# Kernel optimization log

Measured on AMD Instinct MI355X. Metric: run time of the kernel, lower is better.

Reference implementation:

```python
import jax, jax.numpy as jnp
import numpy as np

B, LX, LM, D = 4, 512, 512, 256

def setup_inputs() -> dict:
    key = jax.random.key(0)
    ks = jax.random.split(key, 7)
    s = 1.0 / np.sqrt(D)
    return {
        "x": jax.random.normal(ks[0], (B, LX, D), jnp.float32),
        "memory": jax.random.normal(ks[1], (B, LM, D), jnp.float32),
        "memory_mask": jax.random.randint(ks[2], (B, LM), 0, 2, jnp.int32),
        "W1": jax.random.normal(ks[3], (D, D), jnp.float32) * s,
        "b1": jax.random.normal(ks[4], (D,), jnp.float32) * s,
        "W2": jax.random.normal(ks[5], (D, D), jnp.float32) * s,
        "Wt": jax.random.normal(ks[6], (D,), jnp.float32) * s,
    }

def reference(x, memory, memory_mask, W1, b1, W2, Wt):
    # item1: (B, Lx, D); item2: (B, Lm, D)
    item1 = jnp.einsum("bxd,ed->bxe", x, W1) + b1
    item2 = jnp.einsum("bmd,ed->bme", memory, W2)
    # additive attention: tanh of broadcast sum, then reduce D to scalar logit
    item = item1[:, :, None, :] + item2[:, None, :, :]  # (B, Lx, Lm, D)
    S_logit = jnp.einsum("bxmd,d->bxm", jnp.tanh(item), Wt)
    S_logit = jnp.where(memory_mask[:, None, :] == 0, jnp.float32(-10000.0), S_logit)
    return S_logit
```

## Files before the change

### kernel.cpp

```cpp
#include <hip/hip_runtime.h>

namespace {

constexpr int B = 4, LX = 512, LM = 512, D = 256;
constexpr float KSCALE = 2.8853900817779268f;
constexpr float CLAMP = 7.5f;

typedef __attribute__((ext_vector_type(8))) short short8;
typedef __attribute__((ext_vector_type(4))) float f32x4;
typedef __attribute__((ext_vector_type(2))) float f32x2;

__device__ __forceinline__ unsigned bfbits(float f) {
    unsigned u = __float_as_uint(f);
    u += 0x7FFFu + ((u >> 16) & 1u);
    return u >> 16;
}
__device__ __forceinline__ int pack2(float a, float b) {
    return (int)(bfbits(a) | (bfbits(b) << 16));
}
__device__ __forceinline__ f32x2 up2(unsigned u) {
    f32x2 r;
    r.x = __uint_as_float(u << 16);
    r.y = __uint_as_float(u & 0xFFFF0000u);
    return r;
}
__device__ __forceinline__ unsigned permb(unsigned hi, unsigned lo, unsigned sel) {
    return __builtin_amdgcn_perm(hi, lo, sel);
}

__global__ __launch_bounds__(256) void proj_mfma(
    const float* __restrict__ x, const float* __restrict__ mem,
    const float* __restrict__ W1, const float* __restrict__ b1v,
    const float* __restrict__ W2,
    unsigned short* __restrict__ E1h, unsigned short* __restrict__ E2h)
{
    const int tid = threadIdx.x;
    const int m0c = blockIdx.x * 32;
    const int e0  = blockIdx.y * 64;
    const int z   = m0c >= 2048;
    const int r0  = z ? (m0c - 2048) : m0c;
    const float* __restrict__ A = (z ? mem : x) + (size_t)r0 * D;
    const float* __restrict__ W = z ? W2 : W1;

    __shared__ short sA[32][40];
    __shared__ short sW[64][40];

    const int wid = tid >> 6, lane = tid & 63;
    const int lr = lane & 15, quad = lane >> 4;
    const int g   = wid & 1;
    const int cg0 = (wid >> 1) * 2;
    const int srA = tid >> 3;
    const int scA = (tid & 7) * 4;

    f32x4 acc0 = {0.f, 0.f, 0.f, 0.f};
    f32x4 acc1 = {0.f, 0.f, 0.f, 0.f};

    for (int kc = 0; kc < D; kc += 32) {
        float4 av = *(const float4*)&A[(size_t)srA * D + kc + scA];
        float4 w0 = *(const float4*)&W[(size_t)(e0 + srA) * D + kc + scA];
        float4 w1 = *(const float4*)&W[(size_t)(e0 + 32 + srA) * D + kc + scA];
        __syncthreads();
        *(int2*)&sA[srA][scA]      = make_int2(pack2(av.x, av.y), pack2(av.z, av.w));
        *(int2*)&sW[srA][scA]      = make_int2(pack2(w0.x, w0.y), pack2(w0.z, w0.w));
        *(int2*)&sW[srA + 32][scA] = make_int2(pack2(w1.x, w1.y), pack2(w1.z, w1.w));
        __syncthreads();
        short8 af  = *(const short8*)&sA[g * 16 + lr][quad * 8];
        short8 bf0 = *(const short8*)&sW[cg0 * 16 + lr][quad * 8];
        short8 bf1 = *(const short8*)&sW[cg0 * 16 + 16 + lr][quad * 8];
        acc0 = __builtin_amdgcn_mfma_f32_16x16x32_bf16(af, bf0, acc0, 0, 0, 0);
        acc1 = __builtin_amdgcn_mfma_f32_16x16x32_bf16(af, bf1, acc1, 0, 0, 0);
    }

    const float bias0 = z ? 0.f : b1v[e0 + cg0 * 16 + lr];
    const float bias1 = z ? 0.f : b1v[e0 + cg0 * 16 + 16 + lr];
    const int ec0 = e0 + cg0 * 16 + lr;
#pragma unroll
    for (int reg = 0; reg < 4; ++reg) {
        const int pair = quad * 4 + reg;
        float a0 = KSCALE * (acc0[reg] + bias0);
        float a1 = KSCALE * (acc1[reg] + bias1);
        a0 = fminf(fmaxf(a0, -CLAMP), CLAMP);
        a1 = fminf(fmaxf(a1, -CLAMP), CLAMP);
        const unsigned short e0b = (unsigned short)bfbits(__builtin_amdgcn_exp2f(a0));
        const unsigned short e1b = (unsigned short)bfbits(__builtin_amdgcn_exp2f(a1));
        if (!z) {
            const size_t base = (size_t)((r0 >> 5) * 16 + pair) * 256;
            E1h[(base + ec0) * 2 + g]      = e0b;
            E1h[(base + ec0 + 16) * 2 + g] = e1b;
        } else {
            const int row = r0 + g * 16 + pair;
            E2h[(size_t)row * 256 + ec0]      = e0b;
            E2h[(size_t)row * 256 + ec0 + 16] = e1b;
        }
    }
}

constexpr int RS = 268;
constexpr int C1 = 136;

__global__ __launch_bounds__(256, 4) void tanh_score_kernel(
    const unsigned* __restrict__ E1p, const unsigned* __restrict__ E2u,
    const float* __restrict__ Wt, const int* __restrict__ mask,
    float* __restrict__ out)
{
    const int tid = threadIdx.x;
    const int b   = blockIdx.z;
    const int yb  = blockIdx.y;
    const int T   = yb >> 1;
    const int p0  = (yb & 1) * 8;
    const int bx  = blockIdx.x;

    __shared__ unsigned sA[8 * RS];
    __shared__ unsigned sB[16 * RS];
    __shared__ int scid[LM];
    __shared__ int smsk[LM];
    __shared__ float4 sRed[128];

    const int lane = tid & 63;
    const int wid  = tid >> 6;

    int mvv[8];
#pragma unroll
    for (int c = 0; c < 8; ++c) mvv[c] = mask[b * LM + c * 64 + lane];
    int count = 0, mcount = 0;
#pragma unroll
    for (int c = 0; c < 8; ++c) {
        const bool bit = mvv[c] != 0;
        const unsigned long long bal = __ballot(bit);
        const unsigned long long lt  = (1ull << lane) - 1ull;
        const int pre  = __popcll(bal & lt);
        const int prem = __popcll(~bal & lt);
        if (wid == 0) {
            if (bit) scid[count + pre]   = c * 64 + lane;
            else     smsk[mcount + prem] = c * 64 + lane;
        }
        const int pc = __popcll(bal);
        count  += pc;
        mcount += 64 - pc;
    }

    {
        const int rA = tid >> 5, q2 = tid & 31;
        const unsigned* g =
            E1p + (size_t)((b * 16 + T) * 16 + p0 + rA) * 256 + q2 * 8;
        const int off = rA * RS + q2 * 8 + (q2 >= 16 ? 8 : 0);
        *(uint4*)&sA[off]     = *(const uint4*)(g);
        *(uint4*)&sA[off + 4] = *(const uint4*)(g + 4);
    }

    float sumW = 0.f;
#pragma unroll
    for (int i = 0; i < 256; i += 4) {
        const float4 w = *(const float4*)&Wt[i];
        sumW += (w.x + w.y) + (w.z + w.w);
    }

    __syncthreads();

    const int tx = tid & 15;
    const int ty = (tid >> 4) & 7;
    const int h  = tid >> 7;
    const int hb = h * 128;
    const int ho = h * C1;
    const f32x2 one2 = {1.f, 1.f};

#define SPL(s)  ((f32x2){(s), (s)})
#define FMA2(A_, B_, C_) __builtin_elementwise_fma((A_), (B_), (C_))
#define OCT(BX, accv) { \
    const f32x2 T0 = FMA2(a_[0], BX(0), one2), T1 = FMA2(a_[1], BX(1), one2); \
    const f32x2 T2 = FMA2(a_[2], BX(2), one2), T3 = FMA2(a_[3], BX(3), one2); \
    const f32x2 T4 = FMA2(a_[4], BX(4), one2), T5 = FMA2(a_[5], BX(5), one2); \
    const f32x2 T6 = FMA2(a_[6], BX(6), one2), T7 = FMA2(a_[7], BX(7), one2); \
    const f32x2 L0 = T0 * T1, L1 = T2 * T3, L2 = T4 * T5, L3 = T6 * T7;       \
    const f32x2 Q0 = L0 * L1, Q1 = L2 * L3;                                   \
    const f32x2 den = Q0 * Q1;                                                \
    const f32x2 n0 = FMA2(SPL(wv[0]), T1, SPL(wv[1]) * T0);                   \
    const f32x2 n1 = FMA2(SPL(wv[2]), T3, SPL(wv[3]) * T2);                   \
    const f32x2 n2 = FMA2(SPL(wv[4]), T5, SPL(wv[5]) * T4);                   \
    const f32x2 n3 = FMA2(SPL(wv[6]), T7, SPL(wv[7]) * T6);                   \
    const f32x2 u0 = FMA2(n0, L1, n1 * L0), u1 = FMA2(n2, L3, n3 * L2);       \
    const f32x2 N  = FMA2(u0, Q1, u1 * Q0);                                   \
    f32x2 r; r.x = __builtin_amdgcn_rcpf(den.x);                              \
             r.y = __builtin_amdgcn_rcpf(den.y);                              \
    (accv) = FMA2(N, r, (accv)); }
#define BP(i)  (p_[i])
#define BPS(i) (__builtin_shufflevector(p_[i], p_[i], 1, 0))

    for (int s = bx; s < 16; s += 8) {
        const int m0 = s * 32;
        if (m0 >= count) break;

        {
            const int rB = tid >> 4, q = tid & 15;
            const int clo = min(m0 + rB, count - 1);
            const int chi = min(m0 + rB + 16, count - 1);
            const unsigned* rlo = E2u + (size_t)(b * LM + scid[clo]) * 128 + q * 8;
            const unsigned* rhi = E2u + (size_t)(b * LM + scid[chi]) * 128 + q * 8;
            const uint4 Lo0 = *(const uint4*)(rlo);
            const uint4 Lo1 = *(const uint4*)(rlo + 4);
            const uint4 Hi0 = *(const uint4*)(rhi);
            const uint4 Hi1 = *(const uint4*)(rhi + 4);
            const int ob = rB * RS + q * 16 + (q >= 8 ? 8 : 0);
            uint4 P;
            P.x = permb(Hi0.x, Lo0.x, 0x05040100u); P.y = permb(Hi0.x, Lo0.x, 0x07060302u);
            P.z = permb(Hi0.y, Lo0.y, 0x05040100u); P.w = permb(Hi0.y, Lo0.y, 0x07060302u);
            *(uint4*)&sB[ob] = P;
            P.x = permb(Hi0.z, Lo0.z, 0x05040100u); P.y = permb(Hi0.z, Lo0.z, 0x07060302u);
            P.z = permb(Hi0.w, Lo0.w, 0x05040100u); P.w = permb(Hi0.w, Lo0.w, 0x07060302u);
            *(uint4*)&sB[ob + 4] = P;
            P.x = permb(Hi1.x, Lo1.x, 0x05040100u); P.y = permb(Hi1.x, Lo1.x, 0x07060302u);
            P.z = permb(Hi1.y, Lo1.y, 0x05040100u); P.w = permb(Hi1.y, Lo1.y, 0x07060302u);
            *(uint4*)&sB[ob + 8] = P;
            P.x = permb(Hi1.z, Lo1.z, 0x05040100u); P.y = permb(Hi1.z, Lo1.z, 0x07060302u);
            P.z = permb(Hi1.w, Lo1.w, 0x05040100u); P.w = permb(Hi1.w, Lo1.w, 0x07060302u);
            *(uint4*)&sB[ob + 12] = P;
        }
        __syncthreads();

        f32x2 accs = {0.f, 0.f}, accw = {0.f, 0.f};
#pragma unroll 1
        for (int d = 0; d < 128; d += 8) {
            const uint4 ua0 = *(const uint4*)&sA[ty * RS + ho + d];
            const uint4 ua1 = *(const uint4*)&sA[ty * RS + ho + d + 4];
            const uint4 ub0 = *(const uint4*)&sB[tx * RS + ho + d];
            const uint4 ub1 = *(const uint4*)&sB[tx * RS + ho + d + 4];
            const float4 w0 = *(const float4*)&Wt[hb + d];
            const float4 w1 = *(const float4*)&Wt[hb + d + 4];

            const f32x2 a_[8] = {up2(ua0.x), up2(ua0.y), up2(ua0.z), up2(ua0.w),
                                 up2(ua1.x), up2(ua1.y), up2(ua1.z), up2(ua1.w)};
            const f32x2 p_[8] = {up2(ub0.x), up2(ub0.y), up2(ub0.z), up2(ub0.w),
                                 up2(ub1.x), up2(ub1.y), up2(ub1.z), up2(ub1.w)};
            const float wv[8] = {w0.x, w0.y, w0.z, w0.w, w1.x, w1.y, w1.z, w1.w};

            OCT(BP,  accs)
            OCT(BPS, accw)
        }

        if (h) sRed[ty * 16 + tx] = make_float4(accs.x, accs.y, accw.x, accw.y);
        __syncthreads();
        if (!h) {
            const float4 r = sRed[ty * 16 + tx];
            const int xA = T * 32 + p0 + ty, xB = xA + 16;
            const int col0 = m0 + tx, col1 = m0 + 16 + tx;
            if (col0 < count) {
                const int mo = scid[col0];
                out[((size_t)b * LX + xA) * LM + mo] = sumW - 2.f * (accs.x + r.x);
                out[((size_t)b * LX + xB) * LM + mo] = sumW - 2.f * (accw.y + r.w);
            }
            if (col1 < count) {
                const int mo = scid[col1];
                out[((size_t)b * LX + xA) * LM + mo] = sumW - 2.f * (accw.x + r.z);
                out[((size_t)b * LX + xB) * LM + mo] = sumW - 2.f * (accs.y + r.y);
            }
        }
    }
#undef BP
#undef BPS
#undef OCT
#undef FMA2
#undef SPL

    if (bx == 0) {
        const int xA = T * 32 + p0 + ty, xB = xA + 16;
        const int idx = h * 16 + tx;
        for (int k = idx; k < mcount; k += 32) {
            const int mo = smsk[k];
            out[((size_t)b * LX + xA) * LM + mo] = -10000.f;
            out[((size_t)b * LX + xB) * LM + mo] = -10000.f;
        }
    }
}

}

extern "C" void kernel_launch(void* const* d_in, const int* in_sizes, int n_in,
                              void* d_out, int out_size, void* d_ws, size_t ws_size,
                              hipStream_t stream)
{
    const float* x    = (const float*)d_in[0];
    const float* mem  = (const float*)d_in[1];
    const int*   mask = (const int*)d_in[2];
    const float* W1   = (const float*)d_in[3];
    const float* b1   = (const float*)d_in[4];
    const float* W2   = (const float*)d_in[5];
    const float* Wt   = (const float*)d_in[6];
    float* out = (float*)d_out;

    unsigned*       E1p = (unsigned*)d_ws;
    unsigned short* E2h = (unsigned short*)(E1p + (size_t)(B * LX / 32) * 16 * 256);

    proj_mfma<<<dim3(128, 4), 256, 0, stream>>>(
        x, mem, W1, b1, W2, (unsigned short*)E1p, E2h);

    tanh_score_kernel<<<dim3(8, 32, 4), 256, 0, stream>>>(
        E1p, (const unsigned*)E2h, Wt, mask, out);
}
```

Before: 99.84 us.

## Stage whole K range in LDS for projection and drop bf16 unpack mask

The projection kernel now loads all eight K-chunks of A and W into a larger LDS buffer up front with a single barrier, replacing the per-chunk load/sync/compute loop, so global loads can be issued together and per-iteration barriers disappear. Separately, the bf16 upconversion in the main attention loop skips masking the low half of the high element, which saves one AND per pair but leaves small low-order garbage in the mantissa. The larger LDS footprint per block may lower occupancy of the projection kernel.

```diff
diff --git a/kernel.cpp b/kernel.cpp
--- a/kernel.cpp
+++ b/kernel.cpp
@@ -18,10 +18,10 @@
 __device__ __forceinline__ int pack2(float a, float b) {
     return (int)(bfbits(a) | (bfbits(b) << 16));
 }
-__device__ __forceinline__ f32x2 up2(unsigned u) {
+__device__ __forceinline__ f32x2 up2r(unsigned u) {
     f32x2 r;
     r.x = __uint_as_float(u << 16);
-    r.y = __uint_as_float(u & 0xFFFF0000u);
+    r.y = __uint_as_float(u);
     return r;
 }
 __device__ __forceinline__ unsigned permb(unsigned hi, unsigned lo, unsigned sel) {
@@ -42,8 +42,8 @@
     const float* __restrict__ A = (z ? mem : x) + (size_t)r0 * D;
     const float* __restrict__ W = z ? W2 : W1;
 
-    __shared__ short sA[32][40];
-    __shared__ short sW[64][40];
+    __shared__ short sA[8][32][40];
+    __shared__ short sW[8][64][40];
 
     const int wid = tid >> 6, lane = tid & 63;
     const int lr = lane & 15, quad = lane >> 4;
@@ -52,21 +52,25 @@
     const int srA = tid >> 3;
     const int scA = (tid & 7) * 4;
 
+#pragma unroll
+    for (int kc8 = 0; kc8 < 8; ++kc8) {
+        const int kc = kc8 * 32;
+        const float4 av = *(const float4*)&A[(size_t)srA * D + kc + scA];
+        const float4 w0 = *(const float4*)&W[(size_t)(e0 + srA) * D + kc + scA];
+        const float4 w1 = *(const float4*)&W[(size_t)(e0 + 32 + srA) * D + kc + scA];
+        *(int2*)&sA[kc8][srA][scA]      = make_int2(pack2(av.x, av.y), pack2(av.z, av.w));
+        *(int2*)&sW[kc8][srA][scA]      = make_int2(pack2(w0.x, w0.y), pack2(w0.z, w0.w));
+        *(int2*)&sW[kc8][srA + 32][scA] = make_int2(pack2(w1.x, w1.y), pack2(w1.z, w1.w));
+    }
+    __syncthreads();
+
     f32x4 acc0 = {0.f, 0.f, 0.f, 0.f};
     f32x4 acc1 = {0.f, 0.f, 0.f, 0.f};
-
-    for (int kc = 0; kc < D; kc += 32) {
-        float4 av = *(const float4*)&A[(size_t)srA * D + kc + scA];
-        float4 w0 = *(const float4*)&W[(size_t)(e0 + srA) * D + kc + scA];
-        float4 w1 = *(const float4*)&W[(size_t)(e0 + 32 + srA) * D + kc + scA];
-        __syncthreads();
-        *(int2*)&sA[srA][scA]      = make_int2(pack2(av.x, av.y), pack2(av.z, av.w));
-        *(int2*)&sW[srA][scA]      = make_int2(pack2(w0.x, w0.y), pack2(w0.z, w0.w));
-        *(int2*)&sW[srA + 32][scA] = make_int2(pack2(w1.x, w1.y), pack2(w1.z, w1.w));
-        __syncthreads();
-        short8 af  = *(const short8*)&sA[g * 16 + lr][quad * 8];
-        short8 bf0 = *(const short8*)&sW[cg0 * 16 + lr][quad * 8];
-        short8 bf1 = *(const short8*)&sW[cg0 * 16 + 16 + lr][quad * 8];
+#pragma unroll
+    for (int kc8 = 0; kc8 < 8; ++kc8) {
+        short8 af  = *(const short8*)&sA[kc8][g * 16 + lr][quad * 8];
+        short8 bf0 = *(const short8*)&sW[kc8][cg0 * 16 + lr][quad * 8];
+        short8 bf1 = *(const short8*)&sW[kc8][cg0 * 16 + 16 + lr][quad * 8];
         acc0 = __builtin_amdgcn_mfma_f32_16x16x32_bf16(af, bf0, acc0, 0, 0, 0);
         acc1 = __builtin_amdgcn_mfma_f32_16x16x32_bf16(af, bf1, acc1, 0, 0, 0);
     }
@@ -227,10 +231,10 @@
             const float4 w0 = *(const float4*)&Wt[hb + d];
             const float4 w1 = *(const float4*)&Wt[hb + d + 4];
 
-            const f32x2 a_[8] = {up2(ua0.x), up2(ua0.y), up2(ua0.z), up2(ua0.w),
-                                 up2(ua1.x), up2(ua1.y), up2(ua1.z), up2(ua1.w)};
-            const f32x2 p_[8] = {up2(ub0.x), up2(ub0.y), up2(ub0.z), up2(ub0.w),
-                                 up2(ub1.x), up2(ub1.y), up2(ub1.z), up2(ub1.w)};
+            const f32x2 a_[8] = {up2r(ua0.x), up2r(ua0.y), up2r(ua0.z), up2r(ua0.w),
+                                 up2r(ua1.x), up2r(ua1.y), up2r(ua1.z), up2r(ua1.w)};
+            const f32x2 p_[8] = {up2r(ub0.x), up2r(ub0.y), up2r(ub0.z), up2r(ub0.w),
+                                 up2r(ub1.x), up2r(ub1.y), up2r(ub1.z), up2r(ub1.w)};
             const float wv[8] = {w0.x, w0.y, w0.z, w0.w, w1.x, w1.y, w1.z, w1.w};
 
             OCT(BP,  accs)
```

New measurement: 96.92 us. 1.03x faster.
